# Optimization experiments

Measured on AMD Instinct MI355X. Metric: run time of the kernel, lower is better.

The kernel has to match this reference:

```python
import jax, jax.numpy as jnp
import numpy as np

N, K = 8192, 64          # num pixels (b*h*w), proj_dim
C, M = 19, 10            # num_classes, num_prototype


def setup_inputs() -> dict:
    key = jax.random.key(0)
    k1, k2, k3 = jax.random.split(key, 3)
    x = jax.random.normal(k1, (N, K), dtype=jnp.float32)
    x_var = jax.random.uniform(k2, (N, K), dtype=jnp.float32)  # positive variances
    proto_mean = jax.random.normal(k3, (C, M, K), dtype=jnp.float32) * 0.02  # trunc_normal std=0.02
    proto_var = jnp.ones((C, M, K), dtype=jnp.float32)
    return {"x": x, "x_var": x_var, "proto_mean": proto_mean, "proto_var": proto_var}


def reference(x, x_var, proto_mean, proto_var):
    # MLS similarity: sim = -0.5 * mean_k[ (mu - x)^2 / (sig_x + sig_p) + log(sig_x + sig_p) ]
    pm = proto_mean[:, :, None, :]            # (c, m, 1, k)
    pv = proto_var[:, :, None, :]             # (c, m, 1, k)
    mean_diff = jnp.square(pm - x)            # (c, m, n, k) broadcast
    var_sum = x_var + pv                      # (c, m, n, k)
    sim = mean_diff / var_sum + jnp.log(var_sum)
    sim = -0.5 * jnp.mean(sim, axis=-1)       # (c, m, n)
    return jnp.transpose(sim, (2, 0, 1))      # (n, c, m) == permute(2, 0, 1)
```

## Files before the change

### kernel.cpp

```cpp
#include <hip/hip_runtime.h>

#define NROWS 8192
#define KDIM  64
#define CMDIM 190
#define CMT   10
#define NCT   19

__global__ __launch_bounds__(64)
void probproto_kernel(const float* __restrict__ x,
                      const float* __restrict__ xv,
                      const float* __restrict__ pm,
                      const float* __restrict__ pv,
                      float* __restrict__ out)
{
    const int lane = threadIdx.x;
    const int ct   = blockIdx.x;
    const int n    = blockIdx.y * 64 + lane;

    float xr[KDIM], vr[KDIM];
    const float4* xp = (const float4*)(x  + (size_t)n * KDIM);
    const float4* vp = (const float4*)(xv + (size_t)n * KDIM);
    #pragma unroll
    for (int i = 0; i < KDIM / 4; ++i) {
        float4 a = xp[i], b = vp[i];
        xr[4*i+0] = a.x; xr[4*i+1] = a.y; xr[4*i+2] = a.z; xr[4*i+3] = a.w;
        vr[4*i+0] = b.x; vr[4*i+1] = b.y; vr[4*i+2] = b.z; vr[4*i+3] = b.w;
    }

    float* orow = out + (size_t)n * CMDIM + ct * CMT;

    for (int j = 0; j < CMT; ++j) {
        const float* pmr = pm + (size_t)(ct * CMT + j) * KDIM;
        const float* pvr = pv + (size_t)(ct * CMT + j) * KDIM;

        float q[4] = {0.f, 0.f, 0.f, 0.f};
        float accL = 0.f;
        #pragma unroll
        for (int kc = 0; kc < 4; ++kc) {
            float p[4] = {1.f, 1.f, 1.f, 1.f};
            #pragma unroll
            for (int k8 = 0; k8 < 16; ++k8) {
                int k = kc * 16 + k8;
                float v = vr[k] + pvr[k];
                float d = pmr[k] - xr[k];
                q[k8 & 3] = fmaf(d * d, __builtin_amdgcn_rcpf(v), q[k8 & 3]);
                p[k8 & 3] *= v;
            }
            accL += __log2f((p[0] * p[1]) * (p[2] * p[3]));
        }
        orow[j] = -(((q[0] + q[1]) + (q[2] + q[3]))
                    + 0.69314718055994531f * accL) * (1.0f / 128.0f);
    }
}

extern "C" void kernel_launch(void* const* d_in, const int* in_sizes, int n_in,
                              void* d_out, int out_size, void* d_ws, size_t ws_size,
                              hipStream_t stream) {
    const float* x  = (const float*)d_in[0];
    const float* xv = (const float*)d_in[1];
    const float* pm = (const float*)d_in[2];
    const float* pv = (const float*)d_in[3];
    float* out = (float*)d_out;

    dim3 grid(NCT, NROWS / 64);
    probproto_kernel<<<grid, 64, 0, stream>>>(x, xv, pm, pv, out);
}
```

Measured before the change: 92.43 us.

## Map threads to prototypes and loop over pixel rows for coalesced output

Reassigns work so each thread keeps one prototype's mean and variance in registers while a block iterates over eight pixel rows that are uniform across the block. This turns the previously strided per-thread output writes into coalesced row writes and lets the pixel data be loaded as block-uniform values. Two of the 192 threads per block are idle, and there are fewer blocks in total, which may reduce latency hiding.

```diff
diff --git a/kernel.cpp b/kernel.cpp
--- a/kernel.cpp
+++ b/kernel.cpp
@@ -3,35 +3,37 @@
 #define NROWS 8192
 #define KDIM  64
 #define CMDIM 190
-#define CMT   10
-#define NCT   19
+#define RPB   8
 
-__global__ __launch_bounds__(64)
+__global__ __launch_bounds__(192, 3)
 void probproto_kernel(const float* __restrict__ x,
                       const float* __restrict__ xv,
                       const float* __restrict__ pm,
                       const float* __restrict__ pv,
                       float* __restrict__ out)
 {
-    const int lane = threadIdx.x;
-    const int ct   = blockIdx.x;
-    const int n    = blockIdx.y * 64 + lane;
+    const int t    = threadIdx.x;
+    const int cm   = (t >> 6) * 64 + (t & 63);
+    const int cmc  = cm < CMDIM ? cm : CMDIM - 1;
 
-    float xr[KDIM], vr[KDIM];
-    const float4* xp = (const float4*)(x  + (size_t)n * KDIM);
-    const float4* vp = (const float4*)(xv + (size_t)n * KDIM);
-    #pragma unroll
-    for (int i = 0; i < KDIM / 4; ++i) {
-        float4 a = xp[i], b = vp[i];
-        xr[4*i+0] = a.x; xr[4*i+1] = a.y; xr[4*i+2] = a.z; xr[4*i+3] = a.w;
-        vr[4*i+0] = b.x; vr[4*i+1] = b.y; vr[4*i+2] = b.z; vr[4*i+3] = b.w;
+    float pmr[KDIM], pvr[KDIM];
+    {
+        const float4* pm4 = (const float4*)(pm + (size_t)cmc * KDIM);
+        const float4* pv4 = (const float4*)(pv + (size_t)cmc * KDIM);
+        #pragma unroll
+        for (int i = 0; i < KDIM / 4; ++i) {
+            float4 a = pm4[i], b = pv4[i];
+            pmr[4*i+0] = a.x; pmr[4*i+1] = a.y; pmr[4*i+2] = a.z; pmr[4*i+3] = a.w;
+            pvr[4*i+0] = b.x; pvr[4*i+1] = b.y; pvr[4*i+2] = b.z; pvr[4*i+3] = b.w;
+        }
     }
 
-    float* orow = out + (size_t)n * CMDIM + ct * CMT;
+    const int n0 = blockIdx.x * RPB;
 
-    for (int j = 0; j < CMT; ++j) {
-        const float* pmr = pm + (size_t)(ct * CMT + j) * KDIM;
-        const float* pvr = pv + (size_t)(ct * CMT + j) * KDIM;
+    for (int r = 0; r < RPB; ++r) {
+        const int n = n0 + r;
+        const float* xrow = x  + (size_t)n * KDIM;
+        const float* vrow = xv + (size_t)n * KDIM;
 
         float q[4] = {0.f, 0.f, 0.f, 0.f};
         float accL = 0.f;
@@ -41,15 +43,17 @@
             #pragma unroll
             for (int k8 = 0; k8 < 16; ++k8) {
                 int k = kc * 16 + k8;
-                float v = vr[k] + pvr[k];
-                float d = pmr[k] - xr[k];
+                float v = vrow[k] + pvr[k];
+                float d = xrow[k] - pmr[k];
                 q[k8 & 3] = fmaf(d * d, __builtin_amdgcn_rcpf(v), q[k8 & 3]);
                 p[k8 & 3] *= v;
             }
             accL += __log2f((p[0] * p[1]) * (p[2] * p[3]));
         }
-        orow[j] = -(((q[0] + q[1]) + (q[2] + q[3]))
-                    + 0.69314718055994531f * accL) * (1.0f / 128.0f);
+        float res = -(((q[0] + q[1]) + (q[2] + q[3]))
+                      + 0.69314718055994531f * accL) * (1.0f / 128.0f);
+        if (cm < CMDIM)
+            out[(size_t)n * CMDIM + cm] = res;
     }
 }
 
@@ -62,6 +66,5 @@
     const float* pv = (const float*)d_in[3];
     float* out = (float*)d_out;
 
-    dim3 grid(NCT, NROWS / 64);
-    probproto_kernel<<<grid, 64, 0, stream>>>(x, xv, pm, pv, out);
+    probproto_kernel<<<NROWS / RPB, 192, 0, stream>>>(x, xv, pm, pv, out);
 }
```

Result: slower. 136.0 us (+47.2%).
